# Performance work log

Hardware: AMD Instinct MI355X
Metric: run time of the kernel (lower is better)

## Reference

```python
import jax, jax.numpy as jnp
import numpy as np

HIDDEN = 2048
NUM_HEADS = 16
NUM_KV_HEADS = 4
HEAD_DIM = HIDDEN // NUM_HEADS  # 128
ROPE_WAVELENGTH = 1000000
ROPE_SCALING = 1.0
EPS = 1e-6


def _rotate_half(x):
    half = x.shape[-1] // 2
    return jnp.concatenate([-x[..., half:], x[..., :half]], axis=-1)


def apply_rope(x, positions, max_wavelength, scaling_factor):
    head_dim = x.shape[-1]
    inv_freq = 1.0 / max_wavelength ** (jnp.arange(0, head_dim, 2, dtype=jnp.float32) / head_dim)
    scaled_pos = positions.astype(jnp.float32) / scaling_factor
    freqs = jnp.einsum('t,d->td', scaled_pos, inv_freq)
    emb = jnp.concatenate([freqs, freqs], axis=-1)
    cos = jnp.cos(emb)[None, :, None, :]
    sin = jnp.sin(emb)[None, :, None, :]
    return x * cos + _rotate_half(x) * sin


def rms_norm(x, scale, eps=EPS):
    x32 = x.astype(jnp.float32)
    var = jnp.mean(jnp.square(x32), axis=-1, keepdims=True)
    normed = x32 * jax.lax.rsqrt(var + eps)
    return (normed * scale).astype(x.dtype)


def setup_inputs() -> dict:
    key = jax.random.key(0)
    ks = jax.random.split(key, 8)
    B, T = 2, 2048
    x = jax.random.normal(ks[0], (B, T, HIDDEN), dtype=jnp.float32)
    attention_mask = jnp.ones((B, T, T), dtype=bool)
    s = 1.0 / np.sqrt(HIDDEN)
    Wq = jax.random.normal(ks[1], (HIDDEN, NUM_HEADS, HEAD_DIM), dtype=jnp.float32) * s
    Wk = jax.random.normal(ks[2], (HIDDEN, NUM_KV_HEADS, HEAD_DIM), dtype=jnp.float32) * s
    Wv = jax.random.normal(ks[3], (HIDDEN, NUM_KV_HEADS, HEAD_DIM), dtype=jnp.float32) * s
    q_scale = jnp.ones((HEAD_DIM,), dtype=jnp.float32)
    k_scale = jnp.ones((HEAD_DIM,), dtype=jnp.float32)
    Wo = jax.random.normal(ks[4], (NUM_HEADS, HEAD_DIM, HIDDEN), dtype=jnp.float32) * (1.0 / np.sqrt(HIDDEN))
    return {"x": x, "attention_mask": attention_mask, "Wq": Wq, "Wk": Wk, "Wv": Wv,
            "q_scale": q_scale, "k_scale": k_scale, "Wo": Wo}


def reference(x, attention_mask, Wq, Wk, Wv, q_scale, k_scale, Wo):
    B, T, _ = x.shape
    q = jnp.einsum('btc,chd->bthd', x, Wq)
    k = jnp.einsum('btc,chd->bthd', x, Wk)
    v = jnp.einsum('btc,chd->bthd', x, Wv)
    q = rms_norm(q, q_scale)
    k = rms_norm(k, k_scale)
    positions = jnp.arange(T, dtype=jnp.int32)
    q = apply_rope(q, positions, ROPE_WAVELENGTH, ROPE_SCALING)
    k = apply_rope(k, positions, ROPE_WAVELENGTH, ROPE_SCALING)
    repeats = NUM_HEADS // NUM_KV_HEADS
    k = jnp.repeat(k, repeats, axis=2)
    v = jnp.repeat(v, repeats, axis=2)
    scale = HEAD_DIM ** -0.5
    attn_logits = jnp.einsum('bthd,bshd->bhts', q, k) * scale
    attn_logits = jnp.where(attention_mask[:, None, :, :], attn_logits, -1e30)
    attn = jax.nn.softmax(attn_logits.astype(jnp.float32), axis=-1).astype(x.dtype)
    attn_out = jnp.einsum('bhts,bshd->bthd', attn, v)
    return jnp.einsum('bthd,hdc->btc', attn_out, Wo)
```

## Files before the change

kernel.cpp:

```cpp
#include <hip/hip_runtime.h>

typedef __attribute__((ext_vector_type(4))) float f32x4;
typedef __attribute__((ext_vector_type(16))) float f32x16;
typedef __attribute__((ext_vector_type(8))) short short8;
typedef __attribute__((ext_vector_type(4))) unsigned short us4;
typedef __attribute__((ext_vector_type(2))) unsigned int uint2v;

#define HID 2048
#define T 2048
#define B 2
#define NH 16
#define NKV 4
#define HD 128
#define QKVN 3072

__device__ __forceinline__ unsigned short f2b(float f) {
  union { float f; unsigned u; } v; v.f = f;
  return (unsigned short)((v.u + 0x7fffu + ((v.u >> 16) & 1u)) >> 16);
}

__device__ __forceinline__ void gl_lds16(const unsigned short* g, unsigned short* l) {
  __builtin_amdgcn_global_load_lds((const __attribute__((address_space(1))) void*)g,
                                   (__attribute__((address_space(3))) void*)l, 16, 0, 0);
}

__global__ __launch_bounds__(256) void convert_x(const float* __restrict__ x,
                                                 unsigned short* __restrict__ xb) {
  size_t i = ((size_t)blockIdx.x * 256 + threadIdx.x) * 4;
  float4 v = *(const float4*)(x + i);
  us4 o;
  o.x = f2b(v.x); o.y = f2b(v.y); o.z = f2b(v.z); o.w = f2b(v.w);
  *(us4*)(xb + i) = o;
}

__global__ __launch_bounds__(256) void transpose_conv(const float* __restrict__ src,
                                                      unsigned short* __restrict__ dst,
                                                      int R, int C) {
  __shared__ float tile[32][33];
  int c0 = blockIdx.x * 32, r0 = blockIdx.y * 32;
  int tx = threadIdx.x, ty = threadIdx.y;
#pragma unroll
  for (int i = 0; i < 32; i += 8)
    tile[ty + i][tx] = src[(size_t)(r0 + ty + i) * C + c0 + tx];
  __syncthreads();
#pragma unroll
  for (int i = 0; i < 32; i += 8)
    dst[(size_t)(c0 + ty + i) * R + r0 + tx] = f2b(tile[tx][ty + i]);
}

__global__ __launch_bounds__(256) void transpose_v(const float* __restrict__ qkv,
                                                   unsigned short* __restrict__ Vt) {
  __shared__ float tile[32][33];
  int z = blockIdx.z;
  int b = z >> 2, h = z & 3;
  int t0 = blockIdx.x * 32, d0 = blockIdx.y * 32;
  int tx = threadIdx.x, ty = threadIdx.y;
  const float* src = qkv + (size_t)(b * T) * QKVN + 2560 + h * HD;
#pragma unroll
  for (int i = 0; i < 32; i += 8)
    tile[ty + i][tx] = src[(size_t)(t0 + ty + i) * QKVN + d0 + tx];
  __syncthreads();
  unsigned short* dst = Vt + (size_t)z * HD * T;
#pragma unroll
  for (int i = 0; i < 32; i += 8)
    dst[(size_t)(d0 + ty + i) * T + t0 + tx] = f2b(tile[tx][ty + i]);
}

__global__ __launch_bounds__(256) void gemm_bf16(const unsigned short* __restrict__ A,
                                                 const unsigned short* __restrict__ Bt,
                                                 float* __restrict__ C,
                                                 int M, int N, int K) {
  __shared__ unsigned short As[128 * 32];
  __shared__ unsigned short Bs[128 * 32];
  int tid = threadIdx.x;
  int wave = tid >> 6, lane = tid & 63;
  int quad = lane >> 4, l16 = lane & 15;
  int m0 = blockIdx.y * 128, n0 = blockIdx.x * 128;
  int wm = (wave >> 1) * 64, wn = (wave & 1) * 64;
  f32x4 acc[4][4] = {};

  int lrow = lane >> 2, lcol = (lane & 3) * 8;
  const unsigned short* Ag = A + (size_t)(m0 + wave * 32 + lrow) * K + lcol;
  const unsigned short* Bg = Bt + (size_t)(n0 + wave * 32 + lrow) * K + lcol;
  unsigned short* Asw = As + wave * 1024;
  unsigned short* Bsw = Bs + wave * 1024;

  gl_lds16(Ag, Asw);
  gl_lds16(Ag + (size_t)16 * K, Asw + 512);
  gl_lds16(Bg, Bsw);
  gl_lds16(Bg + (size_t)16 * K, Bsw + 512);

  for (int k0 = 0; k0 < K; k0 += 32) {
    __syncthreads();
    short8 a[4], b[4];
#pragma unroll
    for (int mi = 0; mi < 4; ++mi)
      a[mi] = *(short8*)(&As[(wm + mi * 16 + l16) * 32 + quad * 8]);
#pragma unroll
    for (int ni = 0; ni < 4; ++ni)
      b[ni] = *(short8*)(&Bs[(wn + ni * 16 + l16) * 32 + quad * 8]);
#pragma unroll
    for (int mi = 0; mi < 4; ++mi)
#pragma unroll
      for (int ni = 0; ni < 4; ++ni)
        acc[mi][ni] = __builtin_amdgcn_mfma_f32_16x16x32_bf16(a[mi], b[ni], acc[mi][ni], 0, 0, 0);
    __syncthreads();
    if (k0 + 32 < K) {
      const unsigned short* Ag2 = Ag + k0 + 32;
      const unsigned short* Bg2 = Bg + k0 + 32;
      gl_lds16(Ag2, Asw);
      gl_lds16(Ag2 + (size_t)16 * K, Asw + 512);
      gl_lds16(Bg2, Bsw);
      gl_lds16(Bg2 + (size_t)16 * K, Bsw + 512);
    }
  }
#pragma unroll
  for (int mi = 0; mi < 4; ++mi)
#pragma unroll
    for (int r = 0; r < 4; ++r) {
      int row = m0 + wm + mi * 16 + quad * 4 + r;
      float* cp = C + (size_t)row * N + n0 + wn;
#pragma unroll
      for (int ni = 0; ni < 4; ++ni)
        cp[ni * 16 + l16] = acc[mi][ni][r];
    }
}

__global__ __launch_bounds__(256) void norm_rope(const float* __restrict__ qkv,
                                                 const float* __restrict__ q_scale,
                                                 const float* __restrict__ k_scale,
                                                 unsigned short* __restrict__ Qb,
                                                 unsigned short* __restrict__ Kb) {
  int item = blockIdx.x * 4 + (threadIdx.x >> 6);
  int lane = threadIdx.x & 63;
  int idx = item % 20;
  int bt = item / 20;
  int b = bt >> 11, t = bt & 2047;
  bool isq = idx < 16;
  int h = isq ? idx : idx - 16;
  int col = isq ? idx * HD : HID + h * HD;
  const float* src = qkv + (size_t)bt * QKVN + col;
  float x_lo = src[lane], x_hi = src[lane + 64];
  float ss = x_lo * x_lo + x_hi * x_hi;
#pragma unroll
  for (int off = 32; off > 0; off >>= 1) ss += __shfl_xor(ss, off);
  float inv = rsqrtf(ss * (1.0f / 128.0f) + 1e-6f);
  const float* sc = isq ? q_scale : k_scale;
  float nl = x_lo * inv * sc[lane];
  float nh = x_hi * inv * sc[lane + 64];
  float freq = exp2f(-(float)lane * 0.31143075889569023f);
  float ph = (float)t * freq;
  float cs = cosf(ph), sn = sinf(ph);
  float ol = nl * cs - nh * sn;
  float oh = nh * cs + nl * sn;
  if (isq) { ol *= 0.12751743f; oh *= 0.12751743f; }
  unsigned short* dst = isq ? (Qb + ((size_t)(b * NH + h) * T + t) * HD)
                            : (Kb + ((size_t)(b * NKV + h) * T + t) * HD);
  dst[lane] = f2b(ol);
  dst[lane + 64] = f2b(oh);
}

__global__ __launch_bounds__(256, 2) void attn_kernel(const unsigned short* __restrict__ Qb,
                                                      const unsigned short* __restrict__ Kb,
                                                      const unsigned short* __restrict__ Vt,
                                                      unsigned short* __restrict__ AOb) {
  __shared__ unsigned short Ks[64 * 128];
  __shared__ unsigned short Vs[128 * 64];
  __shared__ float Lred[4][32];
  int b = blockIdx.z, h = blockIdx.y;
  int t0 = blockIdx.x * 128;
  int hk = h >> 2;
  int tid = threadIdx.x, wave = tid >> 6, lane = tid & 63;
  int l31 = lane & 31, hi = lane >> 5;
  const unsigned short* Qh = Qb + (size_t)(b * NH + h) * T * HD;
  const unsigned short* Kh = Kb + (size_t)(b * NKV + hk) * T * HD;
  const unsigned short* Vh = Vt + (size_t)(b * NKV + hk) * HD * T;

  short8 qf[8];
#pragma unroll
  for (int kc = 0; kc < 8; ++kc)
    qf[kc] = *(const short8*)(Qh + (size_t)(t0 + wave * 32 + l31) * HD + kc * 16 + hi * 8);

  f32x16 o[4] = {};
  float l_r = 0.0f;

  int krow4 = tid >> 4, kc4 = tid & 15;
  int kphys = (kc4 ^ (krow4 & 7)) * 8;
  int vrow8 = tid >> 3, vc8 = tid & 7;
  int vphys = (vc8 ^ (vrow8 & 7)) * 8;

  short8 kreg[4], vreg[4];
#pragma unroll
  for (int i = 0; i < 4; ++i) {
    kreg[i] = *(const short8*)(Kh + (size_t)(i * 16 + krow4) * HD + kc4 * 8);
    vreg[i] = *(const short8*)(Vh + (size_t)(i * 32 + vrow8) * T + vc8 * 8);
  }

  int swk = l31 & 7;
  for (int s0 = 0; s0 < T; s0 += 64) {
#pragma unroll
    for (int i = 0; i < 4; ++i) {
      *(short8*)(&Ks[(i * 16 + krow4) * 128 + kphys]) = kreg[i];
      *(short8*)(&Vs[(i * 32 + vrow8) * 64 + vphys]) = vreg[i];
    }
    __syncthreads();
    if (s0 + 64 < T) {
#pragma unroll
      for (int i = 0; i < 4; ++i) {
        kreg[i] = *(const short8*)(Kh + (size_t)(s0 + 64 + i * 16 + krow4) * HD + kc4 * 8);
        vreg[i] = *(const short8*)(Vh + (size_t)(i * 32 + vrow8) * T + s0 + 64 + vc8 * 8);
      }
    }
    f32x16 st[2] = {};
    __builtin_amdgcn_s_setprio(1);
#pragma unroll
    for (int kc = 0; kc < 8; ++kc) {
#pragma unroll
      for (int n = 0; n < 2; ++n) {
        short8 ka = *(short8*)(&Ks[(n * 32 + l31) * 128 + (((2 * kc + hi) ^ swk) * 8)]);
        st[n] = __builtin_amdgcn_mfma_f32_32x32x16_bf16(ka, qf[kc], st[n], 0, 0, 0);
      }
    }
    __builtin_amdgcn_s_setprio(0);
    unsigned pw0[2][4], pw1[2][4];
#pragma unroll
    for (int n = 0; n < 2; ++n)
#pragma unroll
      for (int c = 0; c < 4; ++c) {
        float p0 = exp2f(st[n][c * 4 + 0] - 17.0f);
        float p1 = exp2f(st[n][c * 4 + 1] - 17.0f);
        float p2 = exp2f(st[n][c * 4 + 2] - 17.0f);
        float p3 = exp2f(st[n][c * 4 + 3] - 17.0f);
        l_r += (p0 + p1) + (p2 + p3);
        asm("v_cvt_pk_bf16_f32 %0, %1, %2" : "=v"(pw0[n][c]) : "v"(p0), "v"(p1));
        asm("v_cvt_pk_bf16_f32 %0, %1, %2" : "=v"(pw1[n][c]) : "v"(p2), "v"(p3));
      }
    __builtin_amdgcn_s_setprio(1);
#pragma unroll
    for (int ks = 0; ks < 4; ++ks) {
      int n = ks >> 1, ce = (ks & 1) * 2;
      uint2v r0 = __builtin_amdgcn_permlane32_swap(pw0[n][ce], pw0[n][ce + 1], false, false);
      uint2v r1 = __builtin_amdgcn_permlane32_swap(pw1[n][ce], pw1[n][ce + 1], false, false);
      union { unsigned u[4]; short8 s; } pu;
      pu.u[0] = r0[0]; pu.u[1] = r1[0]; pu.u[2] = r0[1]; pu.u[3] = r1[1];
#pragma unroll
      for (int df = 0; df < 4; ++df) {
        short8 vf = *(short8*)(&Vs[(df * 32 + l31) * 64 + (((2 * ks + hi) ^ swk) * 8)]);
        o[df] = __builtin_amdgcn_mfma_f32_32x32x16_bf16(pu.s, vf, o[df], 0, 0, 0);
      }
    }
    __builtin_amdgcn_s_setprio(0);
    __syncthreads();
  }

  float lt = l_r + __shfl_xor(l_r, 32);
  if (hi == 0) Lred[wave][l31] = 1.0f / lt;
  float linv[16];
#pragma unroll
  for (int reg = 0; reg < 16; ++reg)
    linv[reg] = Lred[wave][(reg & 3) + 8 * (reg >> 2) + 4 * hi];
  int tb = t0 + wave * 32;
#pragma unroll
  for (int df = 0; df < 4; ++df)
#pragma unroll
    for (int reg = 0; reg < 16; ++reg) {
      int q = (reg & 3) + 8 * (reg >> 2) + 4 * hi;
      AOb[((size_t)(b * T) + tb + q) * HID + h * HD + df * 32 + l31] = f2b(o[df][reg] * linv[reg]);
    }
}

extern "C" void kernel_launch(void* const* d_in, const int* in_sizes, int n_in,
                              void* d_out, int out_size, void* d_ws, size_t ws_size,
                              hipStream_t stream) {
  const float* x = (const float*)d_in[0];
  const float* Wq = (const float*)d_in[2];
  const float* Wk = (const float*)d_in[3];
  const float* Wv = (const float*)d_in[4];
  const float* q_scale = (const float*)d_in[5];
  const float* k_scale = (const float*)d_in[6];
  const float* Wo = (const float*)d_in[7];
  float* out = (float*)d_out;

  char* ws = (char*)d_ws;
  const size_t MB = 1024 * 1024;
  float* qkv_f32 = (float*)(ws + 0);
  unsigned short* xb  = (unsigned short*)(ws + 48 * MB);
  unsigned short* AOb = xb;
  unsigned short* Wb  = (unsigned short*)(ws + 64 * MB);
  unsigned short* Wob = (unsigned short*)(ws + 76 * MB);
  unsigned short* Qb  = (unsigned short*)(ws + 84 * MB);
  unsigned short* Kb  = (unsigned short*)(ws + 100 * MB);
  unsigned short* Vtg = (unsigned short*)(ws + 104 * MB);

  dim3 tb32(32, 8);
  convert_x<<<(B * T * HID) / 1024, 256, 0, stream>>>(x, xb);
  transpose_conv<<<dim3(64, 64), tb32, 0, stream>>>(Wq, Wb, HID, 2048);
  transpose_conv<<<dim3(16, 64), tb32, 0, stream>>>(Wk, Wb + (size_t)2048 * HID, HID, 512);
  transpose_conv<<<dim3(16, 64), tb32, 0, stream>>>(Wv, Wb + (size_t)2560 * HID, HID, 512);
  transpose_conv<<<dim3(64, 64), tb32, 0, stream>>>(Wo, Wob, HID, 2048);
  gemm_bf16<<<dim3(QKVN / 128, (B * T) / 128), 256, 0, stream>>>(xb, Wb, qkv_f32, B * T, QKVN, HID);
  norm_rope<<<(B * T * 20) / 4, 256, 0, stream>>>(qkv_f32, q_scale, k_scale, Qb, Kb);
  transpose_v<<<dim3(T / 32, HD / 32, B * NKV), tb32, 0, stream>>>(qkv_f32, Vtg);
  attn_kernel<<<dim3(T / 128, NH, B), 256, 0, stream>>>(Qb, Kb, Vtg, AOb);
  gemm_bf16<<<dim3(HID / 128, (B * T) / 128), 256, 0, stream>>>(AOb, Wob, out, B * T, HID, HID);
}
```

Before: 359.9 us.

## Deepen GEMM K-tile to 64 with XOR-swizzled LDS and workgroup remap

The bf16 GEMM now stages 64-wide K slices in LDS instead of 32, which halves the number of barrier pairs per K loop. Global-to-LDS loads place 16-byte chunks at XOR-swizzled positions so the MFMA operand reads avoid LDS bank conflicts. Workgroup IDs are remapped across eight groups to change which output tiles run together, aiming for better L2 reuse. LDS use doubles, and the swizzle assumes the grid size divides evenly by eight.

```diff
diff --git a/kernel.cpp b/kernel.cpp
--- a/kernel.cpp
+++ b/kernel.cpp
@@ -70,48 +70,58 @@
                                                  const unsigned short* __restrict__ Bt,
                                                  float* __restrict__ C,
                                                  int M, int N, int K) {
-  __shared__ unsigned short As[128 * 32];
-  __shared__ unsigned short Bs[128 * 32];
+  __shared__ unsigned short As[128 * 64];
+  __shared__ unsigned short Bs[128 * 64];
   int tid = threadIdx.x;
   int wave = tid >> 6, lane = tid & 63;
   int quad = lane >> 4, l16 = lane & 15;
-  int m0 = blockIdx.y * 128, n0 = blockIdx.x * 128;
+  int gx = gridDim.x;
+  int nwg = gx * gridDim.y;
+  int bid = blockIdx.y * gx + blockIdx.x;
+  int swz = (bid & 7) * (nwg >> 3) + (bid >> 3);
+  int m0 = (swz / gx) * 128, n0 = (swz % gx) * 128;
   int wm = (wave >> 1) * 64, wn = (wave & 1) * 64;
   f32x4 acc[4][4] = {};
 
-  int lrow = lane >> 2, lcol = (lane & 3) * 8;
-  const unsigned short* Ag = A + (size_t)(m0 + wave * 32 + lrow) * K + lcol;
-  const unsigned short* Bg = Bt + (size_t)(n0 + wave * 32 + lrow) * K + lcol;
-  unsigned short* Asw = As + wave * 1024;
-  unsigned short* Bsw = Bs + wave * 1024;
-
-  gl_lds16(Ag, Asw);
-  gl_lds16(Ag + (size_t)16 * K, Asw + 512);
-  gl_lds16(Bg, Bsw);
-  gl_lds16(Bg + (size_t)16 * K, Bsw + 512);
-
-  for (int k0 = 0; k0 < K; k0 += 32) {
+  int srow = lane >> 3;
+  int schunk = (lane & 7) ^ srow;
+  const unsigned short* Ag = A + (size_t)(m0 + wave * 32 + srow) * K + schunk * 8;
+  const unsigned short* Bg = Bt + (size_t)(n0 + wave * 32 + srow) * K + schunk * 8;
+  unsigned short* Asw = As + wave * 32 * 64;
+  unsigned short* Bsw = Bs + wave * 32 * 64;
+
+#pragma unroll
+  for (int i = 0; i < 4; ++i) {
+    gl_lds16(Ag + (size_t)(i * 8) * K, Asw + i * 8 * 64);
+    gl_lds16(Bg + (size_t)(i * 8) * K, Bsw + i * 8 * 64);
+  }
+
+  for (int k0 = 0; k0 < K; k0 += 64) {
     __syncthreads();
-    short8 a[4], b[4];
-#pragma unroll
-    for (int mi = 0; mi < 4; ++mi)
-      a[mi] = *(short8*)(&As[(wm + mi * 16 + l16) * 32 + quad * 8]);
-#pragma unroll
-    for (int ni = 0; ni < 4; ++ni)
-      b[ni] = *(short8*)(&Bs[(wn + ni * 16 + l16) * 32 + quad * 8]);
-#pragma unroll
-    for (int mi = 0; mi < 4; ++mi)
+#pragma unroll
+    for (int kk = 0; kk < 2; ++kk) {
+      short8 a[4], b[4];
+#pragma unroll
+      for (int mi = 0; mi < 4; ++mi)
+        a[mi] = *(short8*)(&As[(wm + mi * 16 + l16) * 64 + (((kk * 4 + quad) ^ (l16 & 7)) * 8)]);
 #pragma unroll
       for (int ni = 0; ni < 4; ++ni)
-        acc[mi][ni] = __builtin_amdgcn_mfma_f32_16x16x32_bf16(a[mi], b[ni], acc[mi][ni], 0, 0, 0);
+        b[ni] = *(short8*)(&Bs[(wn + ni * 16 + l16) * 64 + (((kk * 4 + quad) ^ (l16 & 7)) * 8)]);
+#pragma unroll
+      for (int mi = 0; mi < 4; ++mi)
+#pragma unroll
+        for (int ni = 0; ni < 4; ++ni)
+          acc[mi][ni] = __builtin_amdgcn_mfma_f32_16x16x32_bf16(a[mi], b[ni], acc[mi][ni], 0, 0, 0);
+    }
     __syncthreads();
-    if (k0 + 32 < K) {
-      const unsigned short* Ag2 = Ag + k0 + 32;
-      const unsigned short* Bg2 = Bg + k0 + 32;
-      gl_lds16(Ag2, Asw);
-      gl_lds16(Ag2 + (size_t)16 * K, Asw + 512);
-      gl_lds16(Bg2, Bsw);
-      gl_lds16(Bg2 + (size_t)16 * K, Bsw + 512);
+    if (k0 + 64 < K) {
+      const unsigned short* Ag2 = Ag + k0 + 64;
+      const unsigned short* Bg2 = Bg + k0 + 64;
+#pragma unroll
+      for (int i = 0; i < 4; ++i) {
+        gl_lds16(Ag2 + (size_t)(i * 8) * K, Asw + i * 8 * 64);
+        gl_lds16(Bg2 + (size_t)(i * 8) * K, Bsw + i * 8 * 64);
+      }
     }
   }
 #pragma unroll
```

Result: slower. 381.4 us (+6.0%).
